# Kernel optimization log

Hardware: AMD Instinct MI355X
Metric: run time of the kernel (lower is better)

## Reference

```python
import jax, jax.numpy as jnp
import numpy as np

NUM_HEADS = 16
HEAD_DIM = 64  # hidden_size 1024 / 16 heads


def setup_inputs() -> dict:
    key = jax.random.key(0)
    ks = jax.random.split(key, 4)
    B, S, H = 2, 2048, 1024
    scale = 0.02
    return {
        "hidden_states": jax.random.normal(ks[0], (B, S, H), jnp.float32),
        "attention_mask": jnp.zeros((B, 1, 1, S), jnp.float32),  # additive mask
        "Wq": jax.random.normal(ks[1], (H, H), jnp.float32) * scale,
        "bq": jnp.zeros((H,), jnp.float32),
        "Wk": jax.random.normal(ks[2], (H, H), jnp.float32) * scale,
        "bk": jnp.zeros((H,), jnp.float32),
        "Wv": jax.random.normal(ks[3], (H, H), jnp.float32) * scale,
        "bv": jnp.zeros((H,), jnp.float32),
    }


def _split_heads(x):
    B, S, H = x.shape
    return x.reshape(B, S, NUM_HEADS, HEAD_DIM).transpose(0, 2, 1, 3)  # [B,h,S,dh]


def reference(hidden_states, attention_mask, Wq, bq, Wk, bk, Wv, bv):
    q = _split_heads(hidden_states @ Wq + bq)
    k = _split_heads(hidden_states @ Wk + bk)
    v = _split_heads(hidden_states @ Wv + bv)
    # scaled dot-product scores [B,h,S,S]
    scores = jnp.einsum("bhqd,bhkd->bhqk", q, k) / np.sqrt(HEAD_DIM).astype(np.float32)
    scores = scores + attention_mask  # additive mask, broadcast [B,1,1,S]
    probs = jax.nn.softmax(scores, axis=-1)  # dropout prob = 0.0
    ctx = jnp.einsum("bhqk,bhkd->bhqd", probs, v)
    B, h, S, dh = ctx.shape
    return ctx.transpose(0, 2, 1, 3).reshape(B, S, h * dh)  # [B,S,hidden]
```

## Files before the change

kernel.cpp:

```cpp
#include <hip/hip_runtime.h>
#include <hip/hip_bf16.h>


typedef __bf16 bf16x8 __attribute__((ext_vector_type(8)));
typedef __bf16 bf16x4 __attribute__((ext_vector_type(4)));
typedef float f32x4 __attribute__((ext_vector_type(4)));

static constexpr int H = 1024;
static constexpr int S = 2048;
static constexpr int NH = 16;
static constexpr int DH = 64;
static constexpr float L2E = 1.4426950408889634f;

#if __has_builtin(__builtin_amdgcn_exp2f)
#define EXP2F(x) __builtin_amdgcn_exp2f(x)
#else
#define EXP2F(x) __builtin_exp2f(x)
#endif

__device__ inline void gll16(const void* g, void* l) {
  __builtin_amdgcn_global_load_lds(
      (const __attribute__((address_space(1))) void*)g,
      (__attribute__((address_space(3))) void*)l, 16, 0, 0);
}

__global__ __launch_bounds__(256) void convert_kernel(
    const float* __restrict__ X, const float* __restrict__ W0,
    const float* __restrict__ W1, const float* __restrict__ W2,
    __bf16* __restrict__ Xb, __bf16* __restrict__ Wt) {
  __shared__ float T[64][65];
  const int bid = blockIdx.x, tid = threadIdx.x;
  if (bid < 2048) {
    size_t i = ((size_t)bid * 256 + tid) * 8;
    float4 f0 = *(const float4*)(X + i);
    float4 f1 = *(const float4*)(X + i + 4);
    bf16x8 o;
    o[0] = (__bf16)f0.x; o[1] = (__bf16)f0.y; o[2] = (__bf16)f0.z; o[3] = (__bf16)f0.w;
    o[4] = (__bf16)f1.x; o[5] = (__bf16)f1.y; o[6] = (__bf16)f1.z; o[7] = (__bf16)f1.w;
    *(bf16x8*)(Xb + i) = o;
    return;
  }
  const int wid = bid - 2048;
  const int z = wid >> 8, t = wid & 255;
  const int k0 = (t >> 4) * 64, n0 = (t & 15) * 64;
  const float* W = z == 0 ? W0 : (z == 1 ? W1 : W2);
  __bf16* Wo = Wt + (size_t)z * H * H;
#pragma unroll
  for (int it = 0; it < 4; ++it) {
    int r = it * 16 + (tid >> 4), c = (tid & 15) * 4;
    *(float4*)&T[r][c] = *(const float4*)&W[(size_t)(k0 + r) * H + n0 + c];
  }
  __syncthreads();
#pragma unroll
  for (int it = 0; it < 4; ++it) {
    int n = it * 16 + (tid >> 4), c0 = (tid & 15) * 4;
    bf16x4 o;
#pragma unroll
    for (int j = 0; j < 4; ++j) o[j] = (__bf16)T[c0 + j][n];
    *(bf16x4*)&Wo[(size_t)(n0 + n) * H + k0 + c0] = o;
  }
}

__global__ __launch_bounds__(256, 3) void qkv_gemm_kernel(
    const __bf16* __restrict__ Xb, const __bf16* __restrict__ Wt,
    const float* __restrict__ bq, const float* __restrict__ bk,
    const float* __restrict__ bv,
    __bf16* __restrict__ Qt, __bf16* __restrict__ K, __bf16* __restrict__ Vt)
{
  __shared__ __bf16 As[128 * 64];
  __shared__ __bf16 Bs[128 * 64];

  const int tid = threadIdx.x, lane = tid & 63, w = tid >> 6;
  const int quad = lane >> 4, l16 = lane & 15;
  const int wsel = blockIdx.x >> 3;
  const int n0 = (blockIdx.x & 7) * 128;
  const int m0 = blockIdx.y * 128;
  const int wr = w & 1, wc = w >> 1;

  const __bf16* Wsel = Wt + (size_t)wsel * H * H;
  const float* bias = wsel == 0 ? bq : (wsel == 1 ? bk : bv);

  const __bf16* aptr[4];
  const __bf16* bptr[4];
#pragma unroll
  for (int i = 0; i < 4; ++i) {
    int s = w * 256 + i * 64 + lane;
    int row = s >> 3, col = s & 7, sc = col ^ (row & 7);
    aptr[i] = Xb + (size_t)(m0 + row) * H + sc * 8;
    bptr[i] = Wsel + (size_t)(n0 + row) * H + sc * 8;
  }

  f32x4 acc[4][4] = {};

  for (int k0 = 0; k0 < H; k0 += 64) {
    __syncthreads();
#pragma unroll
    for (int i = 0; i < 4; ++i) {
      gll16(aptr[i] + k0, &As[(w * 256 + i * 64) * 8]);
      gll16(bptr[i] + k0, &Bs[(w * 256 + i * 64) * 8]);
    }
    __syncthreads();
#pragma unroll
    for (int kc = 0; kc < 2; ++kc) {
      bf16x8 af[4], bfr[4];
#pragma unroll
      for (int t = 0; t < 4; ++t) {
        int ra = wr * 64 + t * 16 + l16;
        af[t] = *(const bf16x8*)&As[ra * 64 + (((kc * 4 + quad) ^ (ra & 7)) * 8)];
        int rb = wc * 64 + t * 16 + l16;
        bfr[t] = *(const bf16x8*)&Bs[rb * 64 + (((kc * 4 + quad) ^ (rb & 7)) * 8)];
      }
#pragma unroll
      for (int t = 0; t < 4; ++t)
#pragma unroll
        for (int u = 0; u < 4; ++u)
          acc[t][u] = __builtin_amdgcn_mfma_f32_16x16x32_bf16(af[t], bfr[u], acc[t][u], 0, 0, 0);
    }
  }

  const float qscale = 0.125f * L2E;
#pragma unroll
  for (int u = 0; u < 4; ++u) {
    int n = n0 + wc * 64 + u * 16 + l16;
    int head = n >> 6, d = n & 63;
    float bias_v = bias[n];
#pragma unroll
    for (int t = 0; t < 4; ++t) {
      int srow = m0 + wr * 64 + t * 16 + quad * 4;
      int b = srow >> 11, si = srow & (S - 1);
      int bh = b * NH + head;
      if (wsel == 1) {
        __bf16* dst = K + ((size_t)bh * S + si) * DH + d;
#pragma unroll
        for (int r = 0; r < 4; ++r)
          dst[(size_t)r * DH] = (__bf16)(acc[t][u][r] + bias_v);
      } else {
        float scl = wsel == 0 ? qscale : 1.0f;
        __bf16* outp = wsel == 0 ? Qt : Vt;
        bf16x4 o;
#pragma unroll
        for (int r = 0; r < 4; ++r) o[r] = (__bf16)((acc[t][u][r] + bias_v) * scl);
        *(bf16x4*)&outp[((size_t)bh * DH + d) * S + si] = o;
      }
    }
  }
}

__global__ __launch_bounds__(512, 4) void attn_kernel(
    const __bf16* __restrict__ Qt, const __bf16* __restrict__ K,
    const __bf16* __restrict__ Vt, const float* __restrict__ mask,
    float* __restrict__ out)
{
  __shared__ __bf16 Ks[128 * 64];
  __shared__ __bf16 Vs[64 * 128];
  __shared__ float  Ms[S];
  __shared__ __bf16 Pb[8][16][128];

  const int tid = threadIdx.x, lane = tid & 63, w = tid >> 6;
  const int quad = lane >> 4, l16 = lane & 15;
  const int bh = blockIdx.y, b = bh >> 4, h = bh & 15;
  const int q0 = blockIdx.x * 128;

  const __bf16* Qb = Qt + (size_t)bh * DH * S;
  const __bf16* Kb = K + (size_t)bh * S * DH;
  const __bf16* Vb = Vt + (size_t)bh * DH * S;
  const float* mb = mask + (size_t)b * S;

  {
    int idx = tid * 4;
    float4 mv = *(const float4*)&mb[idx];
    float4 sv = {mv.x * L2E, mv.y * L2E, mv.z * L2E, mv.w * L2E};
    *(float4*)&Ms[idx] = sv;
  }

  const int q = q0 + w * 16 + l16;
  bf16x8 qf[2];
#pragma unroll
  for (int kc = 0; kc < 2; ++kc)
#pragma unroll
    for (int j = 0; j < 8; ++j)
      qf[kc][j] = Qb[(size_t)(kc * 32 + quad * 8 + j) * S + q];

  bf16x8 ones_frag;
#pragma unroll
  for (int j = 0; j < 8; ++j) ones_frag[j] = (l16 == 0) ? (__bf16)1.0f : (__bf16)0.0f;

  const __bf16* kptr[2];
  const __bf16* vptr[2];
#pragma unroll
  for (int i = 0; i < 2; ++i) {
    int s = w * 128 + i * 64 + lane;
    {
      int row = s >> 3, col = s & 7, sc = col ^ (row & 7);
      kptr[i] = Kb + (size_t)row * DH + sc * 8;
    }
    {
      int row = s >> 4, col = s & 15, sc = col ^ (row & 15);
      vptr[i] = Vb + (size_t)row * S + sc * 8;
    }
  }

  f32x4 o[4] = {};
  f32x4 o4 = {};

  for (int kv0 = 0; kv0 < S; kv0 += 128) {
    __syncthreads();
#pragma unroll
    for (int i = 0; i < 2; ++i) {
      gll16(kptr[i] + (size_t)kv0 * DH, &Ks[(w * 128 + i * 64) * 8]);
      gll16(vptr[i] + kv0, &Vs[(w * 128 + i * 64) * 8]);
    }
    __syncthreads();

#pragma unroll
    for (int t = 0; t < 8; ++t) {
      int rk = t * 16 + l16;
      bf16x8 k0f = *(const bf16x8*)&Ks[rk * 64 + ((quad ^ (rk & 7)) * 8)];
      bf16x8 k1f = *(const bf16x8*)&Ks[rk * 64 + (((4 + quad) ^ (rk & 7)) * 8)];
      float4 m4 = *(const float4*)&Ms[kv0 + t * 16 + quad * 4];
      f32x4 z = {m4.x, m4.y, m4.z, m4.w};
      z = __builtin_amdgcn_mfma_f32_16x16x32_bf16(k0f, qf[0], z, 0, 0, 0);
      f32x4 sc = __builtin_amdgcn_mfma_f32_16x16x32_bf16(k1f, qf[1], z, 0, 0, 0);
      bf16x4 pk;
#pragma unroll
      for (int r = 0; r < 4; ++r) pk[r] = (__bf16)EXP2F(sc[r]);
      int col = t * 16 + quad * 4;
      *(bf16x4*)&Pb[w][l16][(((col >> 3) ^ l16) & 15) * 8 + (col & 7)] = pk;
    }

#pragma unroll
    for (int tt = 0; tt < 4; ++tt) {
      bf16x8 pf = *(const bf16x8*)&Pb[w][l16][(((tt * 4 + quad) ^ l16) & 15) * 8];
#pragma unroll
      for (int u = 0; u < 4; ++u) {
        int d = u * 16 + l16;
        bf16x8 vf = *(const bf16x8*)&Vs[d * 128 + (((4 * tt + quad) ^ l16) * 8)];
        o[u] = __builtin_amdgcn_mfma_f32_16x16x32_bf16(vf, pf, o[u], 0, 0, 0);
      }
      o4 = __builtin_amdgcn_mfma_f32_16x16x32_bf16(ones_frag, pf, o4, 0, 0, 0);
    }
  }

  float l_q = __shfl(o4[0], l16, 64);
  float invl = 1.0f / l_q;
#pragma unroll
  for (int u = 0; u < 4; ++u) {
    float4 st = {o[u][0] * invl, o[u][1] * invl, o[u][2] * invl, o[u][3] * invl};
    *(float4*)&out[((size_t)b * S + q) * H + h * DH + u * 16 + quad * 4] = st;
  }
}

extern "C" void kernel_launch(void* const* d_in, const int* in_sizes, int n_in,
                              void* d_out, int out_size, void* d_ws, size_t ws_size,
                              hipStream_t stream) {
  const float* X    = (const float*)d_in[0];
  const float* mask = (const float*)d_in[1];
  const float* Wq   = (const float*)d_in[2];
  const float* bq   = (const float*)d_in[3];
  const float* Wk   = (const float*)d_in[4];
  const float* bk   = (const float*)d_in[5];
  const float* Wv   = (const float*)d_in[6];
  const float* bv   = (const float*)d_in[7];
  float* out = (float*)d_out;

  const size_t per = (size_t)2 * NH * S * DH;
  __bf16* Qws  = (__bf16*)d_ws;
  __bf16* Kws  = Qws + per;
  __bf16* Vtws = Kws + per;

  __bf16* Xb = (__bf16*)d_out;
  __bf16* Wt = Xb + per;

  convert_kernel<<<2816, 256, 0, stream>>>(X, Wq, Wk, Wv, Xb, Wt);
  qkv_gemm_kernel<<<dim3(24, 32), 256, 0, stream>>>(Xb, Wt, bq, bk, bv,
                                                    Qws, Kws, Vtws);
  attn_kernel<<<dim3(16, 32), 512, 0, stream>>>(Qws, Kws, Vtws, mask, out);
}
```

Baseline: 169.1 us.

## Split attention KV range across two warp groups and merge partial sums

Each block now handles 64 queries instead of 128, and its 8 warps form two groups that each process half of the key/value sequence (split-K). Partial outputs and row sums are combined through shared memory at the end. This doubles the grid to 1024 blocks and shrinks shared memory, so more blocks fit per CU and occupancy rises. The mask is now read from global memory on every tile instead of being staged in LDS, and the merge step adds an extra barrier and an LDS round trip.

```diff
diff --git a/kernel.cpp b/kernel.cpp
--- a/kernel.cpp
+++ b/kernel.cpp
@@ -146,34 +146,28 @@
   }
 }
 
-__global__ __launch_bounds__(512, 4) void attn_kernel(
+__global__ __launch_bounds__(512, 6) void attn_kernel(
     const __bf16* __restrict__ Qt, const __bf16* __restrict__ K,
     const __bf16* __restrict__ Vt, const float* __restrict__ mask,
     float* __restrict__ out)
 {
-  __shared__ __bf16 Ks[128 * 64];
-  __shared__ __bf16 Vs[64 * 128];
-  __shared__ float  Ms[S];
-  __shared__ __bf16 Pb[8][16][128];
+  __shared__ __align__(16) __bf16 Ks[2 * 64 * 64];
+  __shared__ __align__(16) __bf16 Vs[2 * 64 * 64];
+  __shared__ __align__(16) __bf16 Pb[8 * 16 * 64];
 
   const int tid = threadIdx.x, lane = tid & 63, w = tid >> 6;
   const int quad = lane >> 4, l16 = lane & 15;
   const int bh = blockIdx.y, b = bh >> 4, h = bh & 15;
-  const int q0 = blockIdx.x * 128;
+  const int q0 = blockIdx.x * 64;
+  const int g = w >> 2;
+  const int wq = w & 3;
 
   const __bf16* Qb = Qt + (size_t)bh * DH * S;
   const __bf16* Kb = K + (size_t)bh * S * DH;
   const __bf16* Vb = Vt + (size_t)bh * DH * S;
   const float* mb = mask + (size_t)b * S;
 
-  {
-    int idx = tid * 4;
-    float4 mv = *(const float4*)&mb[idx];
-    float4 sv = {mv.x * L2E, mv.y * L2E, mv.z * L2E, mv.w * L2E};
-    *(float4*)&Ms[idx] = sv;
-  }
-
-  const int q = q0 + w * 16 + l16;
+  const int q = q0 + wq * 16 + l16;
   bf16x8 qf[2];
 #pragma unroll
   for (int kc = 0; kc < 2; ++kc)
@@ -185,68 +179,84 @@
 #pragma unroll
   for (int j = 0; j < 8; ++j) ones_frag[j] = (l16 == 0) ? (__bf16)1.0f : (__bf16)0.0f;
 
-  const __bf16* kptr[2];
-  const __bf16* vptr[2];
+  const __bf16* kp[2];
+  const __bf16* vp[2];
 #pragma unroll
   for (int i = 0; i < 2; ++i) {
-    int s = w * 128 + i * 64 + lane;
-    {
-      int row = s >> 3, col = s & 7, sc = col ^ (row & 7);
-      kptr[i] = Kb + (size_t)row * DH + sc * 8;
-    }
-    {
-      int row = s >> 4, col = s & 15, sc = col ^ (row & 15);
-      vptr[i] = Vb + (size_t)row * S + sc * 8;
-    }
+    int s = i * 512 + tid;
+    int gg = s >> 9, row = (s >> 3) & 63, ch = s & 7;
+    kp[i] = Kb + ((size_t)gg * 1024 + row) * DH + (ch ^ (row & 7)) * 8;
+    vp[i] = Vb + (size_t)row * S + gg * 1024 + (ch ^ (row & 7)) * 8;
   }
 
   f32x4 o[4] = {};
   f32x4 o4 = {};
 
-  for (int kv0 = 0; kv0 < S; kv0 += 128) {
-    __syncthreads();
+  for (int it = 0; it < 16; ++it) {
+    __syncthreads();
+    const size_t koff = (size_t)it * 64 * DH;
+    const int voff = it * 64;
 #pragma unroll
     for (int i = 0; i < 2; ++i) {
-      gll16(kptr[i] + (size_t)kv0 * DH, &Ks[(w * 128 + i * 64) * 8]);
-      gll16(vptr[i] + kv0, &Vs[(w * 128 + i * 64) * 8]);
-    }
-    __syncthreads();
-
-#pragma unroll
-    for (int t = 0; t < 8; ++t) {
+      gll16(kp[i] + koff, &Ks[(i * 512 + w * 64) * 8]);
+      gll16(vp[i] + voff, &Vs[(i * 512 + w * 64) * 8]);
+    }
+    __syncthreads();
+
+    const __bf16* KsG = &Ks[g * 512 * 8];
+    const __bf16* VsG = &Vs[g * 512 * 8];
+    const int kvb = g * 1024 + it * 64;
+
+#pragma unroll
+    for (int t = 0; t < 4; ++t) {
       int rk = t * 16 + l16;
-      bf16x8 k0f = *(const bf16x8*)&Ks[rk * 64 + ((quad ^ (rk & 7)) * 8)];
-      bf16x8 k1f = *(const bf16x8*)&Ks[rk * 64 + (((4 + quad) ^ (rk & 7)) * 8)];
-      float4 m4 = *(const float4*)&Ms[kv0 + t * 16 + quad * 4];
-      f32x4 z = {m4.x, m4.y, m4.z, m4.w};
+      bf16x8 k0f = *(const bf16x8*)&KsG[(rk * 8 + (quad ^ (rk & 7))) * 8];
+      bf16x8 k1f = *(const bf16x8*)&KsG[(rk * 8 + ((4 + quad) ^ (rk & 7))) * 8];
+      float4 mv = *(const float4*)&mb[kvb + t * 16 + quad * 4];
+      f32x4 z = {mv.x * L2E, mv.y * L2E, mv.z * L2E, mv.w * L2E};
       z = __builtin_amdgcn_mfma_f32_16x16x32_bf16(k0f, qf[0], z, 0, 0, 0);
       f32x4 sc = __builtin_amdgcn_mfma_f32_16x16x32_bf16(k1f, qf[1], z, 0, 0, 0);
       bf16x4 pk;
 #pragma unroll
       for (int r = 0; r < 4; ++r) pk[r] = (__bf16)EXP2F(sc[r]);
-      int col = t * 16 + quad * 4;
-      *(bf16x4*)&Pb[w][l16][(((col >> 3) ^ l16) & 15) * 8 + (col & 7)] = pk;
-    }
-
-#pragma unroll
-    for (int tt = 0; tt < 4; ++tt) {
-      bf16x8 pf = *(const bf16x8*)&Pb[w][l16][(((tt * 4 + quad) ^ l16) & 15) * 8];
+      int c3 = 2 * t + (quad >> 1);
+      *(bf16x4*)&Pb[(w * 16 + l16) * 64 + ((c3 ^ (l16 & 7)) * 8 + (quad & 1) * 4)] = pk;
+    }
+
+#pragma unroll
+    for (int tt = 0; tt < 2; ++tt) {
+      bf16x8 pf = *(const bf16x8*)&Pb[(w * 16 + l16) * 64 + (((tt * 4 + quad) ^ (l16 & 7)) * 8)];
 #pragma unroll
       for (int u = 0; u < 4; ++u) {
         int d = u * 16 + l16;
-        bf16x8 vf = *(const bf16x8*)&Vs[d * 128 + (((4 * tt + quad) ^ l16) * 8)];
+        bf16x8 vf = *(const bf16x8*)&VsG[(d * 8 + ((tt * 4 + quad) ^ (d & 7))) * 8];
         o[u] = __builtin_amdgcn_mfma_f32_16x16x32_bf16(vf, pf, o[u], 0, 0, 0);
       }
       o4 = __builtin_amdgcn_mfma_f32_16x16x32_bf16(ones_frag, pf, o4, 0, 0, 0);
     }
   }
 
-  float l_q = __shfl(o4[0], l16, 64);
-  float invl = 1.0f / l_q;
-#pragma unroll
-  for (int u = 0; u < 4; ++u) {
-    float4 st = {o[u][0] * invl, o[u][1] * invl, o[u][2] * invl, o[u][3] * invl};
-    *(float4*)&out[((size_t)b * S + q) * H + h * DH + u * 16 + quad * 4] = st;
+  __syncthreads();
+  if (w >= 4) {
+    f32x4* mo = (f32x4*)Ks;
+    int idx = ((w - 4) * 64 + lane) * 4;
+#pragma unroll
+    for (int u = 0; u < 4; ++u) mo[idx + u] = o[u];
+    ((float*)Pb)[(w - 4) * 64 + lane] = o4[0];
+  }
+  __syncthreads();
+  if (w < 4) {
+    f32x4* mo = (f32x4*)Ks;
+    int idx = (w * 64 + lane) * 4;
+#pragma unroll
+    for (int u = 0; u < 4; ++u) o[u] += mo[idx + u];
+    float l_q = __shfl(o4[0], l16, 64) + ((float*)Pb)[w * 64 + l16];
+    float invl = 1.0f / l_q;
+#pragma unroll
+    for (int u = 0; u < 4; ++u) {
+      float4 st = {o[u][0] * invl, o[u][1] * invl, o[u][2] * invl, o[u][3] * invl};
+      *(float4*)&out[((size_t)b * S + q) * H + h * DH + u * 16 + quad * 4] = st;
+    }
   }
 }
 
@@ -274,5 +284,5 @@
   convert_kernel<<<2816, 256, 0, stream>>>(X, Wq, Wk, Wv, Xb, Wt);
   qkv_gemm_kernel<<<dim3(24, 32), 256, 0, stream>>>(Xb, Wt, bq, bk, bv,
                                                     Qws, Kws, Vtws);
-  attn_kernel<<<dim3(16, 32), 512, 0, stream>>>(Qws, Kws, Vtws, mask, out);
-}
+  attn_kernel<<<dim3(32, 32), 512, 0, stream>>>(Qws, Kws, Vtws, mask, out);
+}
```

After: 192.7 us. +14.0%, slower.

## Store Q and K row-major via LDS-transposed epilogue, fold bias into accumulator init

Applied to the files above, without the earlier changes.

Q now uses a [bh,S,DH] row-major layout instead of transposed. The Q and K epilogues stage the output tile through swizzled shared memory so each lane writes contiguous 128-byte rows, replacing the strided scalar and 4-element stores. The bias is preloaded into the accumulators, and the attention kernel reads its Q fragments with single vector loads instead of strided scalar gathers. The K/V async load slot mapping is also reindexed, and the extra sync and LDS round trip add a little epilogue cost.

```diff
diff --git a/kernel.cpp b/kernel.cpp
--- a/kernel.cpp
+++ b/kernel.cpp
@@ -65,10 +65,11 @@
     const __bf16* __restrict__ Xb, const __bf16* __restrict__ Wt,
     const float* __restrict__ bq, const float* __restrict__ bk,
     const float* __restrict__ bv,
-    __bf16* __restrict__ Qt, __bf16* __restrict__ K, __bf16* __restrict__ Vt)
+    __bf16* __restrict__ Q, __bf16* __restrict__ K, __bf16* __restrict__ Vt)
 {
-  __shared__ __bf16 As[128 * 64];
-  __shared__ __bf16 Bs[128 * 64];
+  __shared__ __bf16 smem[2 * 128 * 64];
+  __bf16* As = smem;
+  __bf16* Bs = smem + 128 * 64;
 
   const int tid = threadIdx.x, lane = tid & 63, w = tid >> 6;
   const int quad = lane >> 4, l16 = lane & 15;
@@ -90,7 +91,13 @@
     bptr[i] = Wsel + (size_t)(n0 + row) * H + sc * 8;
   }
 
-  f32x4 acc[4][4] = {};
+  f32x4 acc[4][4];
+#pragma unroll
+  for (int u = 0; u < 4; ++u) {
+    float bv_ = bias[n0 + wc * 64 + u * 16 + l16];
+#pragma unroll
+    for (int t = 0; t < 4; ++t) acc[t][u] = {bv_, bv_, bv_, bv_};
+  }
 
   for (int k0 = 0; k0 < H; k0 += 64) {
     __syncthreads();
@@ -118,36 +125,51 @@
     }
   }
 
-  const float qscale = 0.125f * L2E;
-#pragma unroll
-  for (int u = 0; u < 4; ++u) {
-    int n = n0 + wc * 64 + u * 16 + l16;
-    int head = n >> 6, d = n & 63;
-    float bias_v = bias[n];
-#pragma unroll
-    for (int t = 0; t < 4; ++t) {
-      int srow = m0 + wr * 64 + t * 16 + quad * 4;
-      int b = srow >> 11, si = srow & (S - 1);
-      int bh = b * NH + head;
-      if (wsel == 1) {
-        __bf16* dst = K + ((size_t)bh * S + si) * DH + d;
-#pragma unroll
-        for (int r = 0; r < 4; ++r)
-          dst[(size_t)r * DH] = (__bf16)(acc[t][u][r] + bias_v);
-      } else {
-        float scl = wsel == 0 ? qscale : 1.0f;
-        __bf16* outp = wsel == 0 ? Qt : Vt;
+  const int b = m0 >> 11;
+  if (wsel <= 1) {
+    __syncthreads();
+    __bf16* Tr = smem + w * (64 * 64);
+    const float scl = wsel == 0 ? 0.125f * L2E : 1.0f;
+#pragma unroll
+    for (int t = 0; t < 4; ++t)
+#pragma unroll
+      for (int u = 0; u < 4; ++u)
+#pragma unroll
+        for (int r = 0; r < 4; ++r) {
+          int row = t * 16 + quad * 4 + r;
+          int col = u * 16 + l16;
+          Tr[row * 64 + (((col >> 3) ^ (row & 7)) * 8 + (col & 7))] =
+              (__bf16)(acc[t][u][r] * scl);
+        }
+    const int head = (n0 + wc * 64) >> 6;
+    const int bh = b * NH + head;
+    const int si = (m0 & (S - 1)) + wr * 64 + lane;
+    __bf16* dst = (wsel == 0 ? Q : K) + ((size_t)bh * S + si) * DH;
+#pragma unroll
+    for (int c = 0; c < 8; ++c)
+      *(bf16x8*)&dst[c * 8] =
+          *(const bf16x8*)&Tr[lane * 64 + ((c ^ (lane & 7)) * 8)];
+  } else {
+#pragma unroll
+    for (int u = 0; u < 4; ++u) {
+      int n = n0 + wc * 64 + u * 16 + l16;
+      int head = n >> 6, d = n & 63;
+#pragma unroll
+      for (int t = 0; t < 4; ++t) {
+        int srow = m0 + wr * 64 + t * 16 + quad * 4;
+        int si = srow & (S - 1);
+        int bh = b * NH + head;
         bf16x4 o;
 #pragma unroll
-        for (int r = 0; r < 4; ++r) o[r] = (__bf16)((acc[t][u][r] + bias_v) * scl);
-        *(bf16x4*)&outp[((size_t)bh * DH + d) * S + si] = o;
+        for (int r = 0; r < 4; ++r) o[r] = (__bf16)acc[t][u][r];
+        *(bf16x4*)&Vt[((size_t)bh * DH + d) * S + si] = o;
       }
     }
   }
 }
 
 __global__ __launch_bounds__(512, 4) void attn_kernel(
-    const __bf16* __restrict__ Qt, const __bf16* __restrict__ K,
+    const __bf16* __restrict__ Q, const __bf16* __restrict__ K,
     const __bf16* __restrict__ Vt, const float* __restrict__ mask,
     float* __restrict__ out)
 {
@@ -161,7 +183,7 @@
   const int bh = blockIdx.y, b = bh >> 4, h = bh & 15;
   const int q0 = blockIdx.x * 128;
 
-  const __bf16* Qb = Qt + (size_t)bh * DH * S;
+  const __bf16* Qb = Q + (size_t)bh * S * DH;
   const __bf16* Kb = K + (size_t)bh * S * DH;
   const __bf16* Vb = Vt + (size_t)bh * DH * S;
   const float* mb = mask + (size_t)b * S;
@@ -177,9 +199,7 @@
   bf16x8 qf[2];
 #pragma unroll
   for (int kc = 0; kc < 2; ++kc)
-#pragma unroll
-    for (int j = 0; j < 8; ++j)
-      qf[kc][j] = Qb[(size_t)(kc * 32 + quad * 8 + j) * S + q];
+    qf[kc] = *(const bf16x8*)&Qb[(size_t)q * DH + kc * 32 + quad * 8];
 
   bf16x8 ones_frag;
 #pragma unroll
@@ -189,7 +209,7 @@
   const __bf16* vptr[2];
 #pragma unroll
   for (int i = 0; i < 2; ++i) {
-    int s = w * 128 + i * 64 + lane;
+    int s = i * 512 + tid;
     {
       int row = s >> 3, col = s & 7, sc = col ^ (row & 7);
       kptr[i] = Kb + (size_t)row * DH + sc * 8;
@@ -207,8 +227,8 @@
     __syncthreads();
 #pragma unroll
     for (int i = 0; i < 2; ++i) {
-      gll16(kptr[i] + (size_t)kv0 * DH, &Ks[(w * 128 + i * 64) * 8]);
-      gll16(vptr[i] + kv0, &Vs[(w * 128 + i * 64) * 8]);
+      gll16(kptr[i] + (size_t)kv0 * DH, &Ks[(i * 512 + w * 64) * 8]);
+      gll16(vptr[i] + kv0, &Vs[(i * 512 + w * 64) * 8]);
     }
     __syncthreads();
 
```

Result: no change. 170.3 us (+0.7%).
